# Kernel tuning notes

Hardware: AMD Instinct MI355X
Metric: run time of the kernel (lower is better)

The kernel has to match this reference:

```python
import jax, jax.numpy as jnp
import numpy as np

D = 1024; H = 16; N = 64; F = 4096
B = 1; T = 2048
W_LORA = 64; A_LORA = 64; V_LORA = 32; G_LORA = 128


def rmsnorm(x, w, eps=1e-6):
    x32 = x.astype(jnp.float32)
    var = jnp.mean(x32 * x32, axis=-1, keepdims=True)
    return w * (x32 * jax.lax.rsqrt(var + eps))


def rwkv7_scan(r, w_log, k, v, a, b, state):
    # r,w_log,k,v,a,b: [B,T,H,N]; state: [B,H,N,N] (value dim, key dim)
    decay = jnp.exp(w_log)  # kernel applies exp to the log-decay w = -exp(w_pre)
    def step(S, inp):
        r_t, d_t, k_t, v_t, a_t, b_t = inp  # each [B,H,N]
        sa = jnp.einsum('bhij,bhj->bhi', S, a_t)
        S = S * d_t[:, :, None, :] + sa[..., None] * b_t[:, :, None, :] + v_t[..., None] * k_t[:, :, None, :]
        o_t = jnp.einsum('bhij,bhj->bhi', S, r_t)
        return S, o_t
    seq = tuple(jnp.moveaxis(t, 1, 0) for t in (r, decay, k, v, a, b))  # [T,B,H,N]
    state_f, o = jax.lax.scan(step, state, seq)
    return jnp.moveaxis(o, 0, 1), state_f  # [B,T,H,N], [B,H,N,N]


def setup_inputs() -> dict:
    key = jax.random.key(0)
    ks = iter(jax.random.split(key, 64))
    def nrm(shape, s=1.0):
        return jax.random.normal(next(ks), shape, dtype=jnp.float32) * s
    def uni(shape):
        return jax.random.uniform(next(ks), shape, dtype=jnp.float32)
    WS = 0.02  # weight scale for big matrices
    inp = {
        'x': nrm((B, T, D)),
        'x_prev': nrm((B, D)),
        'v_first': nrm((B, T, D)),
        'state': jnp.zeros((B, H, N, N), jnp.float32),
        'ln1_w': jnp.ones((D,), jnp.float32),
        'ln2_w': jnp.ones((D,), jnp.float32),
        'x_r': uni((1, 1, D)), 'x_w': uni((1, 1, D)), 'x_k': uni((1, 1, D)),
        'x_v': uni((1, 1, D)), 'x_a': uni((1, 1, D)), 'x_g': uni((1, 1, D)),
        'w0': nrm((1, 1, D), 0.5), 'w1': nrm((D, W_LORA), WS), 'w2': nrm((W_LORA, D), WS),
        'a0': nrm((1, 1, D), 0.1), 'a1': nrm((D, A_LORA), WS), 'a2': nrm((A_LORA, D), WS),
        'v0': nrm((1, 1, D), 0.1), 'v1': nrm((D, V_LORA), WS), 'v2': nrm((V_LORA, D), WS),
        'g1': nrm((D, G_LORA), WS), 'g2': nrm((G_LORA, D), WS),
        'k_k': uni((D,)), 'k_a': uni((D,)), 'r_k': nrm((D,), 0.1),
        'R_': nrm((D, D), WS), 'K_': nrm((D, D), WS), 'V_': nrm((D, D), WS), 'O_': nrm((D, D), WS),
        'gate_w': nrm((D, F), WS), 'up_w': nrm((D, F), WS), 'down_w': nrm((F, D), WS),
    }
    return inp


def _block(x, x_prev, v_first, state, ln1_w, ln2_w, x_r, x_w, x_k, x_v, x_a, x_g,
           w0, w1, w2, a0, a1, a2, v0, v1, v2, g1, g2, k_k, k_a, r_k,
           R_, K_, V_, O_, gate_w, up_w, down_w):
    Bx, Tx, _ = x.shape
    xn = rmsnorm(x, ln1_w)  # ln1
    # token shift
    xx = jnp.concatenate([x_prev[:, None, :], xn[:, :-1]], axis=1) - xn
    xr = xn + xx * x_r; xw = xn + xx * x_w; xk = xn + xx * x_k
    xv = xn + xx * x_v; xa = xn + xx * x_a; xg = xn + xx * x_g
    r = xr @ R_
    w_pre = -jax.nn.softplus(-(w0 + jnp.tanh(xw @ w1) @ w2)) - 0.5
    k = xk @ K_
    v = xv @ V_
    a = jax.nn.sigmoid(a0 + (xa @ a1) @ a2)
    g = jax.nn.sigmoid(xg @ g1) @ g2
    kk = (k * k_k).reshape(Bx, Tx, H, N)
    kk = kk / jnp.maximum(jnp.linalg.norm(kk, axis=-1, keepdims=True), 1e-12)
    kk = kk.reshape(Bx, Tx, H * N)
    k = k * (1 + (a - 1) * k_a)
    # layer_id > 0: lerp toward v_first
    v = v + (v_first - v) * jax.nn.sigmoid(v0 + (xv @ v1) @ v2)
    w_log = -jnp.exp(w_pre)  # log-decay passed to the recurrent kernel
    aa = -kk
    bb = kk * a
    hv = lambda t: t.reshape(Bx, Tx, H, N)
    o, state_f = rwkv7_scan(hv(r), hv(w_log), hv(k), hv(v), hv(aa), hv(bb), state)
    o = o.reshape(Bx, Tx, H * N)
    bonus = ((r * k * r_k).reshape(Bx, Tx, H, N).sum(-1, keepdims=True) * v.reshape(Bx, Tx, H, N)).reshape(Bx, Tx, H * N)
    o = o + bonus
    x = x + (o * g) @ O_
    # SwiGLU MLP
    xm = rmsnorm(x, ln2_w)
    x = x + (jax.nn.silu(xm @ gate_w) * (xm @ up_w)) @ down_w
    return x, xn[:, -1], state_f


def reference(x, x_prev, v_first, state, ln1_w, ln2_w, x_r, x_w, x_k, x_v, x_a, x_g,
              w0, w1, w2, a0, a1, a2, v0, v1, v2, g1, g2, k_k, k_a, r_k,
              R_, K_, V_, O_, gate_w, up_w, down_w):
    return _block(x, x_prev, v_first, state, ln1_w, ln2_w, x_r, x_w, x_k, x_v, x_a, x_g,
                  w0, w1, w2, a0, a1, a2, v0, v1, v2, g1, g2, k_k, k_a, r_k,
                  R_, K_, V_, O_, gate_w, up_w, down_w)
```

## Files before the change

kernel.cpp:

```cpp
#include <hip/hip_runtime.h>
#include <math.h>

#define T_ 2048
#define D_ 1024
#define H_ 16
#define N_ 64
#define F_ 4096
#define NCHUNK 32
#define CLEN 64

typedef __attribute__((ext_vector_type(8))) short bf16x8;
typedef __attribute__((ext_vector_type(4))) float f32x4;
typedef __attribute__((address_space(3))) unsigned int lds_u32_t;
typedef __attribute__((address_space(1))) const unsigned int glb_u32_t;

static __device__ __forceinline__ float sigf(float x) { return 1.0f / (1.0f + __expf(-x)); }

static __device__ __forceinline__ ushort f2bf(float f) {
    union { float f; unsigned u; } c; c.f = f;
    unsigned r = (c.u + 0x7FFFu + ((c.u >> 16) & 1u)) >> 16;
    return (ushort)r;
}
static __device__ __forceinline__ float bf2f(ushort h) {
    union { unsigned u; float f; } c; c.u = ((unsigned)h) << 16;
    return c.f;
}

static __device__ __forceinline__ void st4(float* p, float4 v) { *(float4*)p = v; }
static __device__ __forceinline__ void st4(ushort* p, float4 v) {
    ushort4 o; o.x = f2bf(v.x); o.y = f2bf(v.y); o.z = f2bf(v.z); o.w = f2bf(v.w);
    *(ushort4*)p = o;
}

template <typename OutT>
__global__ __launch_bounds__(256) void rmsnorm_kernel(const float* __restrict__ x,
                                                      const float* __restrict__ w,
                                                      OutT* __restrict__ out,
                                                      float* __restrict__ last) {
    const int t = blockIdx.x;
    const int tid = threadIdx.x;
    const float4* xr = (const float4*)(x + (size_t)t * D_);
    float4 v = xr[tid];
    float ss = v.x * v.x + v.y * v.y + v.z * v.z + v.w * v.w;
    ss += __shfl_xor(ss, 1);
    ss += __shfl_xor(ss, 2);
    ss += __shfl_xor(ss, 4);
    ss += __shfl_xor(ss, 8);
    ss += __shfl_xor(ss, 16);
    ss += __shfl_xor(ss, 32);
    __shared__ float red[4];
    if ((tid & 63) == 0) red[tid >> 6] = ss;
    __syncthreads();
    float tot = red[0] + red[1] + red[2] + red[3];
    float scale = rsqrtf(tot * (1.0f / (float)D_) + 1e-6f);
    float4 wv = ((const float4*)w)[tid];
    float4 o;
    o.x = wv.x * v.x * scale;
    o.y = wv.y * v.y * scale;
    o.z = wv.z * v.z * scale;
    o.w = wv.w * v.w * scale;
    st4(out + (size_t)t * D_ + tid * 4, o);
    if (last != nullptr && t == T_ - 1) ((float4*)last)[tid] = o;
}

__global__ __launch_bounds__(256) void shift_kernel(
    const float* __restrict__ xn, const float* __restrict__ x_prev,
    const float* __restrict__ cr, const float* __restrict__ cw, const float* __restrict__ ck,
    const float* __restrict__ cv, const float* __restrict__ ca, const float* __restrict__ cg,
    ushort* __restrict__ xr, ushort* __restrict__ xw, ushort* __restrict__ xk,
    ushort* __restrict__ xv, ushort* __restrict__ xa, ushort* __restrict__ xg) {
    const int i = blockIdx.x * 256 + threadIdx.x;
    const int t = i >> 8, j = i & 255;
    const float4* xn4 = (const float4*)xn;
    float4 cur = xn4[i];
    float4 prev = (t == 0) ? ((const float4*)x_prev)[j] : xn4[i - 256];
    float4 xx;
    xx.x = prev.x - cur.x;
    xx.y = prev.y - cur.y;
    xx.z = prev.z - cur.z;
    xx.w = prev.w - cur.w;
#define APPLY(dst, c)                                   \
    {                                                   \
        float4 cc = ((const float4*)c)[j];              \
        float4 o;                                       \
        o.x = cur.x + xx.x * cc.x;                      \
        o.y = cur.y + xx.y * cc.y;                      \
        o.z = cur.z + xx.z * cc.z;                      \
        o.w = cur.w + xx.w * cc.w;                      \
        st4(dst + (size_t)i * 4, o);                    \
    }
    APPLY(xr, cr)
    APPLY(xw, cw)
    APPLY(xk, ck)
    APPLY(xv, cv)
    APPLY(xa, ca)
    APPLY(xg, cg)
#undef APPLY
}

struct TDesc { const float* in; ushort* out; int K, N, off; };
struct TPack { TDesc d[15]; };

__global__ __launch_bounds__(256) void transpose_cast_multi(TPack p) {
    __shared__ float tile[32][33];
    const int bid = blockIdx.x;
    int di = 0;
#pragma unroll
    for (int i = 1; i < 15; i++)
        if (bid >= p.d[i].off) di = i;
    const TDesc d = p.d[di];
    const int local = bid - d.off;
    const int nt = d.N >> 5;
    const int bx = local % nt, by = local / nt;
    const int tx = threadIdx.x & 31, ty = threadIdx.x >> 5;
    const int n0 = bx * 32, k0 = by * 32;
#pragma unroll
    for (int i = 0; i < 4; i++)
        tile[ty + i * 8][tx] = d.in[(size_t)(k0 + ty + i * 8) * d.N + n0 + tx];
    __syncthreads();
#pragma unroll
    for (int i = 0; i < 4; i++)
        d.out[(size_t)(n0 + ty + i * 8) * d.K + k0 + tx] = f2bf(tile[tx][ty + i * 8]);
}

template <typename OutT>
__global__ __launch_bounds__(256) void mfma_gemm(
    const ushort* __restrict__ A, const ushort* __restrict__ BT, OutT* __restrict__ C,
    const float* res, int M, int Ntot, int K, int epi) {
    __shared__ ushort As[2][128 * 32];
    __shared__ ushort Bs[2][128 * 32];
    const int tid = threadIdx.x;
    const int wave = tid >> 6, lane = tid & 63;
    const int wr = wave >> 1, wc = wave & 1;
    const int lrow = lane & 15, quad = lane >> 4;
    const int m0 = blockIdx.y * 128, n0 = blockIdx.x * 128;
    const int srow = lane >> 2;
    const int scol = (lane & 3) << 3;

    f32x4 acc[4][4] = {};

    auto stage = [&](int buf, int kk) {
#pragma unroll
        for (int j = 0; j < 2; j++) {
            const int chunk = 2 * wave + j;
            const ushort* ga = A + (size_t)(m0 + chunk * 16 + srow) * K + kk + scol;
            __builtin_amdgcn_global_load_lds((glb_u32_t*)ga,
                                             (lds_u32_t*)&As[buf][chunk * 512], 16, 0, 0);
            const int brow = n0 + chunk * 16 + srow;
            if (brow < Ntot) {
                const ushort* gb = BT + (size_t)brow * K + kk + scol;
                __builtin_amdgcn_global_load_lds((glb_u32_t*)gb,
                                                 (lds_u32_t*)&Bs[buf][chunk * 512], 16, 0, 0);
            }
        }
    };

    stage(0, 0);
    __syncthreads();
    int cur = 0;
    for (int k0 = 0; k0 < K; k0 += 32) {
        if (k0 + 32 < K) stage(cur ^ 1, k0 + 32);
        bf16x8 af[4], bfr[4];
#pragma unroll
        for (int mi = 0; mi < 4; mi++)
            af[mi] = *(const bf16x8*)&As[cur][(wr * 64 + mi * 16 + lrow) * 32 + quad * 8];
#pragma unroll
        for (int ni = 0; ni < 4; ni++)
            bfr[ni] = *(const bf16x8*)&Bs[cur][(wc * 64 + ni * 16 + lrow) * 32 + quad * 8];
#pragma unroll
        for (int mi = 0; mi < 4; mi++)
#pragma unroll
            for (int ni = 0; ni < 4; ni++)
                acc[mi][ni] = __builtin_amdgcn_mfma_f32_16x16x32_bf16(af[mi], bfr[ni], acc[mi][ni], 0, 0, 0);
        __syncthreads();
        cur ^= 1;
    }

#pragma unroll
    for (int mi = 0; mi < 4; mi++) {
#pragma unroll
        for (int r = 0; r < 4; r++) {
            const int row = m0 + wr * 64 + mi * 16 + quad * 4 + r;
#pragma unroll
            for (int ni = 0; ni < 4; ni++) {
                const int col = n0 + wc * 64 + ni * 16 + lrow;
                if (col < Ntot) {
                    const size_t idx = (size_t)row * Ntot + col;
                    float val = acc[mi][ni][r];
                    if (epi == 1) val += res[idx];
                    if constexpr (sizeof(OutT) == 2) C[idx] = (OutT)f2bf(val);
                    else C[idx] = (OutT)val;
                }
            }
        }
    }
}

struct MMDesc {
    const ushort* A; const ushort* BT;
    float* Cf; ushort* Cb;
    const float* res; const float* res2; const float* bias;
    int Ntot, K, epi;
};
template <int NZ>
struct MMPack { MMDesc d[NZ]; };

template <int NZ>
__global__ __launch_bounds__(256) void mfma_gemm_multi(MMPack<NZ> p) {
    const MMDesc d = p.d[blockIdx.z];
    const int n0 = blockIdx.x * 128;
    if (n0 >= d.Ntot) return;
    __shared__ ushort As[2][128 * 32];
    __shared__ ushort Bs[2][128 * 32];
    const int tid = threadIdx.x;
    const int wave = tid >> 6, lane = tid & 63;
    const int wr = wave >> 1, wc = wave & 1;
    const int lrow = lane & 15, quad = lane >> 4;
    const int m0 = blockIdx.y * 128;
    const int srow = lane >> 2;
    const int scol = (lane & 3) << 3;
    const int K = d.K, Ntot = d.Ntot;

    f32x4 acc[4][4] = {};

    auto stage = [&](int buf, int kk) {
#pragma unroll
        for (int j = 0; j < 2; j++) {
            const int chunk = 2 * wave + j;
            const ushort* ga = d.A + (size_t)(m0 + chunk * 16 + srow) * K + kk + scol;
            __builtin_amdgcn_global_load_lds((glb_u32_t*)ga,
                                             (lds_u32_t*)&As[buf][chunk * 512], 16, 0, 0);
            const int brow = n0 + chunk * 16 + srow;
            if (brow < Ntot) {
                const ushort* gb = d.BT + (size_t)brow * K + kk + scol;
                __builtin_amdgcn_global_load_lds((glb_u32_t*)gb,
                                                 (lds_u32_t*)&Bs[buf][chunk * 512], 16, 0, 0);
            }
        }
    };

    stage(0, 0);
    __syncthreads();
    int cur = 0;
    for (int k0 = 0; k0 < K; k0 += 32) {
        if (k0 + 32 < K) stage(cur ^ 1, k0 + 32);
        bf16x8 af[4], bfr[4];
#pragma unroll
        for (int mi = 0; mi < 4; mi++)
            af[mi] = *(const bf16x8*)&As[cur][(wr * 64 + mi * 16 + lrow) * 32 + quad * 8];
#pragma unroll
        for (int ni = 0; ni < 4; ni++)
            bfr[ni] = *(const bf16x8*)&Bs[cur][(wc * 64 + ni * 16 + lrow) * 32 + quad * 8];
#pragma unroll
        for (int mi = 0; mi < 4; mi++)
#pragma unroll
            for (int ni = 0; ni < 4; ni++)
                acc[mi][ni] = __builtin_amdgcn_mfma_f32_16x16x32_bf16(af[mi], bfr[ni], acc[mi][ni], 0, 0, 0);
        __syncthreads();
        cur ^= 1;
    }

#pragma unroll
    for (int mi = 0; mi < 4; mi++) {
#pragma unroll
        for (int r = 0; r < 4; r++) {
            const int row = m0 + wr * 64 + mi * 16 + quad * 4 + r;
#pragma unroll
            for (int ni = 0; ni < 4; ni++) {
                const int col = n0 + wc * 64 + ni * 16 + lrow;
                if (col < Ntot) {
                    const size_t idx = (size_t)row * Ntot + col;
                    float val = acc[mi][ni][r];
                    switch (d.epi) {
                        case 3: val = tanhf(val); break;
                        case 4: val = sigf(val); break;
                        case 5: val = sigf(d.bias[col] + val); break;
                        case 6: val = __expf(-0.60653065971263342f * sigf(d.bias[col] + val)); break;
                        case 7: {
                            float vr = d.res[idx];
                            val = vr + (d.res2[idx] - vr) * sigf(d.bias[col] + val);
                        } break;
                        default: break;
                    }
                    if (d.Cb) d.Cb[idx] = f2bf(val);
                    else d.Cf[idx] = val;
                }
            }
        }
    }
}

__global__ __launch_bounds__(256) void kk_kernel(float* __restrict__ k,
                                                 const float* __restrict__ a_sig,
                                                 const float* __restrict__ k_k,
                                                 const float* __restrict__ k_a,
                                                 float* __restrict__ kk,
                                                 float* __restrict__ mb) {
    const int b = blockIdx.x * 4 + (threadIdx.x >> 6);
    const int t = b >> 4, h = b & 15;
    const int lane = threadIdx.x & 63;
    const size_t idx = (size_t)t * D_ + h * N_ + lane;
    const int wi = h * N_ + lane;
    const float kraw = k[idx];
    const float kv = kraw * k_k[wi];
    float ss = kv * kv;
    ss += __shfl_xor(ss, 1);
    ss += __shfl_xor(ss, 2);
    ss += __shfl_xor(ss, 4);
    ss += __shfl_xor(ss, 8);
    ss += __shfl_xor(ss, 16);
    ss += __shfl_xor(ss, 32);
    const float nrm = fmaxf(sqrtf(ss), 1e-12f);
    const float kkn = kv / nrm;
    kk[idx] = kkn;
    mb[idx] = -kkn * a_sig[idx];
    k[idx] = kraw * (1.0f + (a_sig[idx] - 1.0f) * k_a[wi]);
}

#define FOR16(M) M(0) M(1) M(2) M(3) M(4) M(5) M(6) M(7) \
                 M(8) M(9) M(10) M(11) M(12) M(13) M(14) M(15)

__global__ __launch_bounds__(64, 1) void scan_pass1(
    const float* __restrict__ gR, const float* __restrict__ gD, const float* __restrict__ gK,
    const float* __restrict__ gV, const float* __restrict__ gKK, const float* __restrict__ gMB,
    float* __restrict__ Pbuf, float* __restrict__ Lbuf,
    float* __restrict__ zbuf, float* __restrict__ olbuf) {
    const int bid = blockIdx.x;
    const bool isp = bid >= NCHUNK * H_;
    const int sub = isp ? bid - NCHUNK * H_ : bid;
    const int h = sub & 15;
    const int c = sub >> 4;
    const int lane = threadIdx.x;
    const int hb = h * N_;
    const int t0 = c * CLEN;
    const int tend = t0 + CLEN - 1;

    __shared__ __align__(16) unsigned char ring[2 * 2048];

    const int rsel = lane >> 4;
    const int sub4 = (lane & 15) << 2;
    const float* p1 = (rsel == 0 ? gR : rsel == 1 ? gD : rsel == 2 ? gK : gKK)
                      + (size_t)t0 * D_ + hb + sub4;
    const float* p2 = (rsel == 1 ? gV : gMB) + (size_t)t0 * D_ + hb + sub4;

    const float fid = isp ? 1.0f : 0.0f;
#define DECL(q) f32x4 s##q = {(lane == 4 * q + 0) ? fid : 0.0f, \
                              (lane == 4 * q + 1) ? fid : 0.0f, \
                              (lane == 4 * q + 2) ? fid : 0.0f, \
                              (lane == 4 * q + 3) ? fid : 0.0f};
    FOR16(DECL)
#undef DECL

    float* __restrict__ dotOut = isp ? zbuf : olbuf;

    float4 r0a, r0b, r1a, r1b, r2a, r2b, r3a, r3b;

#define LOADQ(qa, qb, tt) {                                                  \
        const size_t _adv = (size_t)((tt) - t0) * D_;                        \
        qa = *(const float4*)(p1 + _adv);                                    \
        qb = *(const float4*)(p2 + _adv); }
#define WRITEQ(sl, qa, qb) {                                                 \
        *(float4*)(ring + (sl) * 2048 + lane * 16) = qa;                     \
        *(float4*)(ring + (sl) * 2048 + 1024 + lane * 16) = qb; }
#define PA(q) { const f32x4 kk4 = sKKr[q]; sacc += s##q * kk4; }
#define PB(q) {                                                   \
        const f32x4 d4 = sDr[q];                                  \
        const f32x4 k4 = sKr[q];                                  \
        const f32x4 m4 = sMBr[q];                                 \
        const f32x4 r4 = sRr[q];                                  \
        s##q = s##q * d4 + (m4 * sap + k4 * vv);                  \
        oacc += s##q * r4;                                        \
    }
#define COMPUTE(sl, tt) {                                                    \
        const unsigned char* sb = (const unsigned char*)ring + (sl) * 2048;  \
        const f32x4* sRr = (const f32x4*)(sb);                               \
        const f32x4* sDr = (const f32x4*)(sb + 256);                         \
        const f32x4* sKr = (const f32x4*)(sb + 512);                         \
        const f32x4* sKKr = (const f32x4*)(sb + 768);                        \
        const f32x4* sMBr = (const f32x4*)(sb + 1024);                       \
        const float* sVr = (const float*)(sb + 1280);                        \
        f32x4 sacc = {0.f, 0.f, 0.f, 0.f};                                   \
        FOR16(PA)                                                            \
        const float sap = (sacc.x + sacc.y) + (sacc.z + sacc.w);             \
        const float vv = isp ? 0.0f : sVr[lane];                             \
        f32x4 oacc = {0.f, 0.f, 0.f, 0.f};                                   \
        FOR16(PB)                                                            \
        dotOut[(size_t)(tt) * D_ + hb + lane] =                              \
            (oacc.x + oacc.y) + (oacc.z + oacc.w); }

    LOADQ(r0a, r0b, t0)
    LOADQ(r1a, r1b, t0 + 1)
    LOADQ(r2a, r2b, t0 + 2)
    LOADQ(r3a, r3b, t0 + 3)
    WRITEQ(0, r0a, r0b)

    for (int t = t0; t < t0 + CLEN; t += 4) {
        WRITEQ(1, r1a, r1b)
        LOADQ(r0a, r0b, (t + 4 > tend ? tend : t + 4))
        COMPUTE(0, t)
        WRITEQ(0, r2a, r2b)
        LOADQ(r1a, r1b, (t + 5 > tend ? tend : t + 5))
        COMPUTE(1, t + 1)
        WRITEQ(1, r3a, r3b)
        LOADQ(r2a, r2b, (t + 6 > tend ? tend : t + 6))
        COMPUTE(0, t + 2)
        WRITEQ(0, r0a, r0b)
        LOADQ(r3a, r3b, (t + 7 > tend ? tend : t + 7))
        COMPUTE(1, t + 3)
    }
#undef COMPUTE
#undef PB
#undef PA
#undef WRITEQ
#undef LOADQ

    float* __restrict__ sd = isp ? Pbuf : Lbuf;
    const size_t base = ((size_t)c * 16 + h) * 4096 + (size_t)lane * 64;
#define ST(q) *(f32x4*)(sd + base + 4 * q) = s##q;
    FOR16(ST)
#undef ST
}

__global__ __launch_bounds__(256) void scan_combine(
    const float* __restrict__ state_in, const float* __restrict__ Pbuf,
    const float* __restrict__ Lbuf, float* __restrict__ SstT, float* __restrict__ state_out) {
    const int h = blockIdx.x >> 2, rg = blockIdx.x & 3;
    const int tid = threadIdx.x;
    const int i = tid >> 4, j4 = (tid & 15) << 2;
    const int gi = rg * 16 + i;
    __shared__ float Sl[16][68];
    __shared__ float Pl[64][68];

    float4 sv = *(const float4*)(state_in + (size_t)h * 4096 + gi * 64 + j4);
    *(float4*)&Sl[i][j4] = sv;
    __syncthreads();

    for (int c = 0; c < NCHUNK; c++) {
        const size_t cb = ((size_t)c * 16 + h) * 4096;
        float4 scur = *(const float4*)&Sl[i][j4];
        SstT[cb + (size_t)(j4 + 0) * 64 + gi] = scur.x;
        SstT[cb + (size_t)(j4 + 1) * 64 + gi] = scur.y;
        SstT[cb + (size_t)(j4 + 2) * 64 + gi] = scur.z;
        SstT[cb + (size_t)(j4 + 3) * 64 + gi] = scur.w;
#pragma unroll
        for (int q = 0; q < 4; q++) {
            const int pr = (tid >> 4) + q * 16;
            *(float4*)&Pl[pr][j4] = *(const float4*)(Pbuf + cb + (size_t)pr * 64 + j4);
        }
        __syncthreads();
        float4 acc = *(const float4*)(Lbuf + cb + (size_t)gi * 64 + j4);
#pragma unroll 8
        for (int m = 0; m < 64; m++) {
            const float smv = Sl[i][m];
            const float4 p4 = *(const float4*)&Pl[m][j4];
            acc.x = fmaf(smv, p4.x, acc.x);
            acc.y = fmaf(smv, p4.y, acc.y);
            acc.z = fmaf(smv, p4.z, acc.z);
            acc.w = fmaf(smv, p4.w, acc.w);
        }
        __syncthreads();
        *(float4*)&Sl[i][j4] = acc;
        __syncthreads();
    }
    *(float4*)(state_out + (size_t)h * 4096 + gi * 64 + j4) = *(const float4*)&Sl[i][j4];
}

__global__ __launch_bounds__(256) void scan_fix(
    const float* __restrict__ zbuf, const float* __restrict__ olbuf,
    const float* __restrict__ SstT, float* __restrict__ o) {
    const int tg = blockIdx.x >> 4, h = blockIdx.x & 15;
    const int hb = h * N_;
    const int tid = threadIdx.x;
    const int tok = tid >> 4, i4 = (tid & 15) << 2;
    const int tbase = tg * 16;
    const int c = tbase >> 6;
    __shared__ float zl[16][68];
    __shared__ float Sl[64][68];

    *(float4*)&zl[tok][i4] = *(const float4*)(zbuf + (size_t)(tbase + tok) * D_ + hb + i4);
    const size_t cb = ((size_t)c * 16 + h) * 4096;
#pragma unroll
    for (int q = 0; q < 4; q++) {
        const int jr = (tid >> 4) + q * 16;
        *(float4*)&Sl[jr][i4] = *(const float4*)(SstT + cb + (size_t)jr * 64 + i4);
    }
    __syncthreads();
    float4 acc = *(const float4*)(olbuf + (size_t)(tbase + tok) * D_ + hb + i4);
#pragma unroll 8
    for (int j = 0; j < 64; j++) {
        const float zv = zl[tok][j];
        const float4 p4 = *(const float4*)&Sl[j][i4];
        acc.x = fmaf(zv, p4.x, acc.x);
        acc.y = fmaf(zv, p4.y, acc.y);
        acc.z = fmaf(zv, p4.z, acc.z);
        acc.w = fmaf(zv, p4.w, acc.w);
    }
    *(float4*)(o + (size_t)(tbase + tok) * D_ + hb + i4) = acc;
}

__global__ __launch_bounds__(256) void bonus_kernel(const float* __restrict__ o,
                                                    const float* __restrict__ r,
                                                    const float* __restrict__ k,
                                                    const float* __restrict__ v,
                                                    const float* __restrict__ g,
                                                    const float* __restrict__ r_k,
                                                    ushort* __restrict__ og) {
    const int b = blockIdx.x * 4 + (threadIdx.x >> 6);
    const int t = b >> 4, h = b & 15;
    const int lane = threadIdx.x & 63;
    const size_t idx = (size_t)t * D_ + h * N_ + lane;
    float c = r[idx] * k[idx] * r_k[h * N_ + lane];
    c += __shfl_xor(c, 1);
    c += __shfl_xor(c, 2);
    c += __shfl_xor(c, 4);
    c += __shfl_xor(c, 8);
    c += __shfl_xor(c, 16);
    c += __shfl_xor(c, 32);
    const float on = o[idx] + c * v[idx];
    og[idx] = f2bf(on * g[idx]);
}

__global__ __launch_bounds__(256) void mulz_kernel(const ushort* __restrict__ Z,
                                                   ushort* __restrict__ Hb) {
    const int idx = blockIdx.x * 256 + threadIdx.x;
    const int t = idx >> 10;
    const int j = (idx & 1023) << 2;
    const ushort4 zg = *(const ushort4*)(Z + (size_t)t * 8192 + j);
    const ushort4 zu = *(const ushort4*)(Z + (size_t)t * 8192 + 4096 + j);
    ushort4 o;
    float g0 = bf2f(zg.x), g1 = bf2f(zg.y), g2 = bf2f(zg.z), g3 = bf2f(zg.w);
    o.x = f2bf(g0 * sigf(g0) * bf2f(zu.x));
    o.y = f2bf(g1 * sigf(g1) * bf2f(zu.y));
    o.z = f2bf(g2 * sigf(g2) * bf2f(zu.z));
    o.w = f2bf(g3 * sigf(g3) * bf2f(zu.w));
    *(ushort4*)(Hb + (size_t)t * 4096 + j) = o;
}

extern "C" void kernel_launch(void* const* d_in, const int* in_sizes, int n_in,
                              void* d_out, int out_size, void* d_ws, size_t ws_size,
                              hipStream_t stream) {
    const float* x      = (const float*)d_in[0];
    const float* x_prev = (const float*)d_in[1];
    const float* v_first= (const float*)d_in[2];
    const float* state  = (const float*)d_in[3];
    const float* ln1_w  = (const float*)d_in[4];
    const float* ln2_w  = (const float*)d_in[5];
    const float* x_r    = (const float*)d_in[6];
    const float* x_w    = (const float*)d_in[7];
    const float* x_k    = (const float*)d_in[8];
    const float* x_v    = (const float*)d_in[9];
    const float* x_a    = (const float*)d_in[10];
    const float* x_g    = (const float*)d_in[11];
    const float* w0     = (const float*)d_in[12];
    const float* w1     = (const float*)d_in[13];
    const float* w2     = (const float*)d_in[14];
    const float* a0     = (const float*)d_in[15];
    const float* a1     = (const float*)d_in[16];
    const float* a2     = (const float*)d_in[17];
    const float* v0     = (const float*)d_in[18];
    const float* v1     = (const float*)d_in[19];
    const float* v2     = (const float*)d_in[20];
    const float* g1     = (const float*)d_in[21];
    const float* g2     = (const float*)d_in[22];
    const float* k_k    = (const float*)d_in[23];
    const float* k_a    = (const float*)d_in[24];
    const float* r_k    = (const float*)d_in[25];
    const float* R_     = (const float*)d_in[26];
    const float* K_     = (const float*)d_in[27];
    const float* V_     = (const float*)d_in[28];
    const float* O_     = (const float*)d_in[29];
    const float* gate_w = (const float*)d_in[30];
    const float* up_w   = (const float*)d_in[31];
    const float* down_w = (const float*)d_in[32];

    float* ws = (float*)d_ws;
    const size_t U = (size_t)T_ * D_;
    float* u_r  = ws;
    float* u_k  = ws + 1 * U;
    float* u_v  = ws + 2 * U;
    float* u_dc = ws + 3 * U;
    float* u_kk = ws + 4 * U;
    float* u_mb = ws + 5 * U;
    float* u_g  = ws + 6 * U;
    float* u_ao = ws + 7 * U;
    ushort* XB = (ushort*)(ws + 8 * U);
    const size_t TD = U;
    ushort* XR = XB + 0 * TD;
    ushort* XW = XB + 1 * TD;
    ushort* XK = XB + 2 * TD;
    ushort* XV = XB + 3 * TD;
    ushort* XA = XB + 4 * TD;
    ushort* XG = XB + 5 * TD;
    ushort* XM   = XB + 0 * TD;
    ushort* OG   = XB + 1 * TD;
    ushort* Hbuf = XB + 2 * TD;
    ushort* Zbuf = (ushort*)ws;
    float* Pbuf  = u_ao;
    float* Lbuf  = (float*)XB;
    float* zbuf  = (float*)(XB + 2 * TD);
    float* olbuf = (float*)(XB + 4 * TD);
    float* SstT  = u_dc;
    float* obuf  = u_kk;
    ushort* WT = (ushort*)(ws + 11 * U);
    const size_t DD = (size_t)D_ * D_;
    const size_t DF = (size_t)D_ * F_;
    ushort* WTR = WT;
    ushort* WTK = WTR + DD;
    ushort* WTV = WTK + DD;
    ushort* WTO = WTV + DD;
    ushort* WTG = WTO + DD;
    ushort* WTU = WTG + DF;
    ushort* WTD = WTU + DF;
    ushort* WTw1 = WTD + DF;
    ushort* WTw2 = WTw1 + 64 * 1024;
    ushort* WTa1 = WTw2 + 64 * 1024;
    ushort* WTa2 = WTa1 + 64 * 1024;
    ushort* WTv1 = WTa2 + 64 * 1024;
    ushort* WTv2 = WTv1 + 32 * 1024;
    ushort* WTg1 = WTv2 + 32 * 1024;
    ushort* WTg2 = WTg1 + 128 * 1024;
    ushort* Lw = WTg2 + 128 * 1024;
    ushort* La = Lw + (size_t)T_ * 64;
    ushort* Lv = La + (size_t)T_ * 64;
    ushort* Lg = Lv + (size_t)T_ * 32;

    float* out_x = (float*)d_out;
    float* out_xn_last = out_x + (size_t)T_ * D_;
    float* out_state = out_xn_last + D_;

    TPack tp;
    int toff = 0, ti = 0;
    auto addT = [&](const float* in, ushort* out, int K, int N) {
        tp.d[ti].in = in; tp.d[ti].out = out; tp.d[ti].K = K; tp.d[ti].N = N; tp.d[ti].off = toff;
        toff += (N / 32) * (K / 32); ++ti;
    };
    addT(R_, WTR, D_, D_);
    addT(K_, WTK, D_, D_);
    addT(V_, WTV, D_, D_);
    addT(O_, WTO, D_, D_);
    addT(gate_w, WTG, D_, F_);
    addT(up_w, WTU, D_, F_);
    addT(down_w, WTD, F_, D_);
    addT(w1, WTw1, D_, 64);
    addT(w2, WTw2, 64, D_);
    addT(a1, WTa1, D_, 64);
    addT(a2, WTa2, 64, D_);
    addT(v1, WTv1, D_, 32);
    addT(v2, WTv2, 32, D_);
    addT(g1, WTg1, D_, 128);
    addT(g2, WTg2, 128, D_);
    transpose_cast_multi<<<toff, 256, 0, stream>>>(tp);

    rmsnorm_kernel<float><<<T_, 256, 0, stream>>>(x, ln1_w, out_x, out_xn_last);
    shift_kernel<<<T_, 256, 0, stream>>>(out_x, x_prev, x_r, x_w, x_k, x_v, x_a, x_g,
                                         XR, XW, XK, XV, XA, XG);
    auto mkmm = [](const ushort* A, const ushort* BT, float* Cf, ushort* Cb,
                   const float* res, const float* res2, const float* bias,
                   int Ntot, int K, int epi) {
        MMDesc m{A, BT, Cf, Cb, res, res2, bias, Ntot, K, epi};
        return m;
    };
    MMPack<7> pa;
    pa.d[0] = mkmm(XR, WTR, u_r, nullptr, nullptr, nullptr, nullptr, D_, D_, 0);
    pa.d[1] = mkmm(XK, WTK, u_k, nullptr, nullptr, nullptr, nullptr, D_, D_, 0);
    pa.d[2] = mkmm(XV, WTV, u_v, nullptr, nullptr, nullptr, nullptr, D_, D_, 0);
    pa.d[3] = mkmm(XW, WTw1, nullptr, Lw, nullptr, nullptr, nullptr, 64,  D_, 3);
    pa.d[4] = mkmm(XA, WTa1, nullptr, La, nullptr, nullptr, nullptr, 64,  D_, 0);
    pa.d[5] = mkmm(XV, WTv1, nullptr, Lv, nullptr, nullptr, nullptr, 32,  D_, 0);
    pa.d[6] = mkmm(XG, WTg1, nullptr, Lg, nullptr, nullptr, nullptr, 128, D_, 4);
    mfma_gemm_multi<7><<<dim3(8, 16, 7), 256, 0, stream>>>(pa);
    MMPack<4> pb;
    pb.d[0] = mkmm(Lw, WTw2, u_dc, nullptr, nullptr, nullptr, w0, D_, 64,  6);
    pb.d[1] = mkmm(La, WTa2, u_ao, nullptr, nullptr, nullptr, a0, D_, 64,  5);
    pb.d[2] = mkmm(Lv, WTv2, u_v,  nullptr, u_v, v_first,     v0, D_, 32,  7);
    pb.d[3] = mkmm(Lg, WTg2, u_g,  nullptr, nullptr, nullptr, nullptr, D_, 128, 0);
    mfma_gemm_multi<4><<<dim3(8, 16, 4), 256, 0, stream>>>(pb);
    kk_kernel<<<T_ * H_ / 4, 256, 0, stream>>>(u_k, u_ao, k_k, k_a, u_kk, u_mb);
    scan_pass1<<<NCHUNK * H_ * 2, 64, 0, stream>>>(u_r, u_dc, u_k, u_v, u_kk, u_mb,
                                                   Pbuf, Lbuf, zbuf, olbuf);
    scan_combine<<<H_ * 4, 256, 0, stream>>>(state, Pbuf, Lbuf, SstT, out_state);
    scan_fix<<<(T_ / 16) * H_, 256, 0, stream>>>(zbuf, olbuf, SstT, obuf);
    bonus_kernel<<<T_ * H_ / 4, 256, 0, stream>>>(obuf, u_r, u_k, u_v, u_g, r_k, OG);
    mfma_gemm<float><<<dim3(8, 16), 256, 0, stream>>>(OG, WTO, out_x, x, T_, D_, D_, 1);
    rmsnorm_kernel<ushort><<<T_, 256, 0, stream>>>(out_x, ln2_w, XM, nullptr);
    mfma_gemm<ushort><<<dim3(64, 16), 256, 0, stream>>>(XM, WTG, Zbuf, nullptr, T_, 2 * F_, D_, 0);
    mulz_kernel<<<(T_ * (F_ / 4)) / 256, 256, 0, stream>>>(Zbuf, Hbuf);
    mfma_gemm<float><<<dim3(8, 16), 256, 0, stream>>>(Hbuf, WTD, out_x, out_x, T_, D_, F_, 1);
}
```

Measured before the change: 661.4 us.

## Split-K the O and down projections with fused residual-add rmsnorm reduction

```diff
diff --git a/kernel.cpp b/kernel.cpp
--- a/kernel.cpp
+++ b/kernel.cpp
@@ -63,6 +63,52 @@
     if (last != nullptr && t == T_ - 1) ((float4*)last)[tid] = o;
 }
 
+__global__ __launch_bounds__(256) void rmsnorm_reduce2(
+    const float* __restrict__ x, const float* __restrict__ p0, const float* __restrict__ p1,
+    const float* __restrict__ w, float* __restrict__ resid_out, ushort* __restrict__ xm) {
+    const int t = blockIdx.x;
+    const int tid = threadIdx.x;
+    const size_t base = (size_t)t * D_ + tid * 4;
+    float4 v = *(const float4*)(x + base);
+    float4 a = *(const float4*)(p0 + base);
+    float4 b = *(const float4*)(p1 + base);
+    v.x += a.x + b.x; v.y += a.y + b.y; v.z += a.z + b.z; v.w += a.w + b.w;
+    st4(resid_out + base, v);
+    float ss = v.x * v.x + v.y * v.y + v.z * v.z + v.w * v.w;
+    ss += __shfl_xor(ss, 1);
+    ss += __shfl_xor(ss, 2);
+    ss += __shfl_xor(ss, 4);
+    ss += __shfl_xor(ss, 8);
+    ss += __shfl_xor(ss, 16);
+    ss += __shfl_xor(ss, 32);
+    __shared__ float red[4];
+    if ((tid & 63) == 0) red[tid >> 6] = ss;
+    __syncthreads();
+    float tot = red[0] + red[1] + red[2] + red[3];
+    float scale = rsqrtf(tot * (1.0f / (float)D_) + 1e-6f);
+    float4 wv = ((const float4*)w)[tid];
+    float4 o;
+    o.x = wv.x * v.x * scale;
+    o.y = wv.y * v.y * scale;
+    o.z = wv.z * v.z * scale;
+    o.w = wv.w * v.w * scale;
+    st4(xm + base, o);
+}
+
+__global__ __launch_bounds__(256) void add4_kernel(float* __restrict__ out,
+                                                   const float* __restrict__ p,
+                                                   int n4slice) {
+    const int i = blockIdx.x * 256 + threadIdx.x;
+    const float4* p4 = (const float4*)p;
+    float4 o = ((const float4*)out)[i];
+    float4 a = p4[i], b = p4[i + n4slice], c = p4[i + 2 * n4slice], d = p4[i + 3 * n4slice];
+    o.x += (a.x + b.x) + (c.x + d.x);
+    o.y += (a.y + b.y) + (c.y + d.y);
+    o.z += (a.z + b.z) + (c.z + d.z);
+    o.w += (a.w + b.w) + (c.w + d.w);
+    ((float4*)out)[i] = o;
+}
+
 __global__ __launch_bounds__(256) void shift_kernel(
     const float* __restrict__ xn, const float* __restrict__ x_prev,
     const float* __restrict__ cr, const float* __restrict__ cw, const float* __restrict__ ck,
@@ -123,17 +169,25 @@
         d.out[(size_t)(n0 + ty + i * 8) * d.K + k0 + tx] = f2bf(tile[tx][ty + i * 8]);
 }
 
-template <typename OutT>
+template <typename OutT, bool PARTIAL>
 __global__ __launch_bounds__(256) void mfma_gemm(
     const ushort* __restrict__ A, const ushort* __restrict__ BT, OutT* __restrict__ C,
-    const float* res, int M, int Ntot, int K, int epi) {
+    const float* res, int M, int Ntot, int K, int klen, int epi) {
     __shared__ ushort As[2][128 * 32];
     __shared__ ushort Bs[2][128 * 32];
     const int tid = threadIdx.x;
     const int wave = tid >> 6, lane = tid & 63;
     const int wr = wave >> 1, wc = wave & 1;
     const int lrow = lane & 15, quad = lane >> 4;
-    const int m0 = blockIdx.y * 128, n0 = blockIdx.x * 128;
+    int bx = blockIdx.x, by = blockIdx.y;
+    if (gridDim.x == 8 && gridDim.y == 16) {
+        const int bid = by * 8 + bx;
+        const int k = bid & 7, i = bid >> 3;
+        bx = ((k & 1) << 2) + (i & 3);
+        by = ((k >> 1) << 2) + (i >> 2);
+    }
+    const int m0 = by * 128, n0 = bx * 128;
+    const int kbase = blockIdx.z * klen;
     const int srow = lane >> 2;
     const int scol = (lane & 3) << 3;
 
@@ -155,11 +209,11 @@
         }
     };
 
-    stage(0, 0);
+    stage(0, kbase);
     __syncthreads();
     int cur = 0;
-    for (int k0 = 0; k0 < K; k0 += 32) {
-        if (k0 + 32 < K) stage(cur ^ 1, k0 + 32);
+    for (int k0 = kbase; k0 < kbase + klen; k0 += 32) {
+        if (k0 + 32 < kbase + klen) stage(cur ^ 1, k0 + 32);
         bf16x8 af[4], bfr[4];
 #pragma unroll
         for (int mi = 0; mi < 4; mi++)
@@ -176,6 +230,7 @@
         cur ^= 1;
     }
 
+    const size_t zoff = PARTIAL ? (size_t)blockIdx.z * M * Ntot : 0;
 #pragma unroll
     for (int mi = 0; mi < 4; mi++) {
 #pragma unroll
@@ -187,9 +242,13 @@
                 if (col < Ntot) {
                     const size_t idx = (size_t)row * Ntot + col;
                     float val = acc[mi][ni][r];
-                    if (epi == 1) val += res[idx];
-                    if constexpr (sizeof(OutT) == 2) C[idx] = (OutT)f2bf(val);
-                    else C[idx] = (OutT)val;
+                    if constexpr (PARTIAL) {
+                        ((float*)C)[idx + zoff] = val;
+                    } else {
+                        if (epi == 1) val += res[idx];
+                        if constexpr (sizeof(OutT) == 2) C[idx] = (OutT)f2bf(val);
+                        else C[idx] = (OutT)val;
+                    }
                 }
             }
         }
@@ -595,6 +654,8 @@
     ushort* OG   = XB + 1 * TD;
     ushort* Hbuf = XB + 2 * TD;
     ushort* Zbuf = (ushort*)ws;
+    float* Opart = u_mb;
+    float* Dpart = ws;
     float* Pbuf  = u_ao;
     float* Lbuf  = (float*)XB;
     float* zbuf  = (float*)(XB + 2 * TD);
@@ -681,9 +742,13 @@
     scan_combine<<<H_ * 4, 256, 0, stream>>>(state, Pbuf, Lbuf, SstT, out_state);
     scan_fix<<<(T_ / 16) * H_, 256, 0, stream>>>(zbuf, olbuf, SstT, obuf);
     bonus_kernel<<<T_ * H_ / 4, 256, 0, stream>>>(obuf, u_r, u_k, u_v, u_g, r_k, OG);
-    mfma_gemm<float><<<dim3(8, 16), 256, 0, stream>>>(OG, WTO, out_x, x, T_, D_, D_, 1);
-    rmsnorm_kernel<ushort><<<T_, 256, 0, stream>>>(out_x, ln2_w, XM, nullptr);
-    mfma_gemm<ushort><<<dim3(64, 16), 256, 0, stream>>>(XM, WTG, Zbuf, nullptr, T_, 2 * F_, D_, 0);
+    mfma_gemm<float, true><<<dim3(8, 16, 2), 256, 0, stream>>>(
+        OG, WTO, Opart, nullptr, T_, D_, D_, 512, 0);
+    rmsnorm_reduce2<<<T_, 256, 0, stream>>>(x, Opart, Opart + U, ln2_w, out_x, XM);
+    mfma_gemm<ushort, false><<<dim3(64, 16), 256, 0, stream>>>(
+        XM, WTG, Zbuf, nullptr, T_, 2 * F_, D_, D_, 0);
     mulz_kernel<<<(T_ * (F_ / 4)) / 256, 256, 0, stream>>>(Zbuf, Hbuf);
-    mfma_gemm<float><<<dim3(8, 16), 256, 0, stream>>>(Hbuf, WTD, out_x, out_x, T_, D_, F_, 1);
-}
+    mfma_gemm<float, true><<<dim3(8, 16, 4), 256, 0, stream>>>(
+        Hbuf, WTD, Dpart, nullptr, T_, D_, F_, 1024, 0);
+    add4_kernel<<<(int)(U / 4 / 256), 256, 0, stream>>>(out_x, Dpart, (int)(U / 4));
+}
```

Measured after the change: 594.4 us. 10.1% less time.
